# Kernel tuning notes

Measured on AMD Instinct MI355X. Metric: run time of the kernel, lower is better.

Reference implementation:

```python
import jax, jax.numpy as jnp
import numpy as np

DIM = 768      # model dim (c_s)
C_PAIR = 128   # pair channels (c_z)
H = 16         # heads
C = DIM // H   # per-head dim (48)
INF = 1e8
EPS = 1e-5


def _ln(x, w=None, b=None):
    mu = jnp.mean(x, axis=-1, keepdims=True)
    var = jnp.mean(jnp.square(x - mu), axis=-1, keepdims=True)
    y = (x - mu) * jax.lax.rsqrt(var + EPS)
    if w is not None:
        y = y * w
    if b is not None:
        y = y + b
    return y


def setup_inputs() -> dict:
    key = jax.random.key(0)
    ks = jax.random.split(key, 12)
    B, S, N = 1, 2, 1024
    sd = 1.0 / np.sqrt(DIM)
    return {
        "single_repr": jax.random.normal(ks[0], (B, S, N, DIM), jnp.float32),
        "single_proj": jax.random.normal(ks[1], (B, S, N, DIM), jnp.float32),
        "pair_repr": jax.random.normal(ks[2], (B, N, N, C_PAIR), jnp.float32),
        "mask": jnp.ones((B, N), jnp.float32),
        # AdaLN params: LN(a) has no affine; LN(s) is scale-only; gate Linear + skip LinearNoBias
        "adaln_s_w": jnp.ones((DIM,), jnp.float32),
        "adaln_gate_w": (jax.random.normal(ks[3], (DIM, DIM), jnp.float32) * sd),
        "adaln_gate_b": jnp.zeros((DIM,), jnp.float32),
        "adaln_skip_w": (jax.random.normal(ks[4], (DIM, DIM), jnp.float32) * sd),
        # Attention params (q/k/v no bias, sigmoid gate linear, output linear)
        "wq": jax.random.normal(ks[5], (DIM, DIM), jnp.float32) * sd,
        "wk": jax.random.normal(ks[6], (DIM, DIM), jnp.float32) * sd,
        "wv": jax.random.normal(ks[7], (DIM, DIM), jnp.float32) * sd,
        "w_gate": jax.random.normal(ks[8], (DIM, DIM), jnp.float32) * sd,
        "b_gate": jnp.ones((DIM,), jnp.float32),
        "wo": jax.random.normal(ks[9], (DIM, DIM), jnp.float32) * sd,
        "bo": jnp.zeros((DIM,), jnp.float32),
        # proj_pair_bias: LayerNorm(c_pair) + LinearNoBias(c_pair, H)
        "pair_ln_w": jnp.ones((C_PAIR,), jnp.float32),
        "pair_ln_b": jnp.zeros((C_PAIR,), jnp.float32),
        "w_pair": jax.random.normal(ks[10], (C_PAIR, H), jnp.float32) / np.sqrt(C_PAIR),
        # output gating linear (bias initialized to -2 as in the module)
        "w_out": jax.random.normal(ks[11], (DIM, DIM), jnp.float32) * sd,
        "b_out": jnp.full((DIM,), -2.0, jnp.float32),
    }


def reference(single_repr, single_proj, pair_repr, mask,
              adaln_s_w, adaln_gate_w, adaln_gate_b, adaln_skip_w,
              wq, wk, wv, w_gate, b_gate, wo, bo,
              pair_ln_w, pair_ln_b, w_pair, w_out, b_out):
    B, S, N, _ = single_repr.shape
    # AdaLN input gating: a = sigmoid(Lin(LN_scale(s))) * LN(a) + LinNoBias(LN_scale(s))
    a = _ln(single_repr)
    s = _ln(single_proj, adaln_s_w)
    a = jax.nn.sigmoid(s @ adaln_gate_w + adaln_gate_b) * a + s @ adaln_skip_w
    # Biases: mask_bias [B,1,1,1,N]; pair_bias [B,1,H,N,N]
    mask_bias = (INF * (mask - 1.0))[:, None, None, None, :]
    pair_bias = _ln(pair_repr, pair_ln_w, pair_ln_b) @ w_pair      # [B,N,N,H]
    pair_bias = jnp.transpose(pair_bias, (0, 3, 1, 2))[:, None]    # [B,1,H,N,N]
    # Multi-head attention with fused biases
    q = (a @ wq).reshape(B, S, N, H, C)
    k = (a @ wk).reshape(B, S, N, H, C)
    v = (a @ wv).reshape(B, S, N, H, C)
    scale = 1.0 / np.sqrt(C)
    scores = jnp.einsum('bsqhc,bskhc->bshqk', q, k) * scale + mask_bias + pair_bias
    attn = jax.nn.softmax(scores, axis=-1)
    o = jnp.einsum('bshqk,bskhc->bsqhc', attn, v).reshape(B, S, N, DIM)
    # sigmoid gating on attention output, then output projection
    o = o * jax.nn.sigmoid(a @ w_gate + b_gate)
    o = o @ wo + bo
    # final sigmoid output gating (input_gating=True)
    out = jax.nn.sigmoid(o @ w_out + b_out) * o
    return out
```

## Files before the change

### kernel.cpp

```cpp
#include <hip/hip_runtime.h>

#define NROWS 2048
#define NN    1024
#define DIMM  768
#define HEADS 16
#define CH    48
#define CPAIR 128

typedef unsigned short u16;
typedef unsigned int   u32;
typedef __attribute__((ext_vector_type(8))) short short8;
typedef __attribute__((ext_vector_type(4))) float f32x4;

__device__ __forceinline__ float sigm(float x){ return 1.0f/(1.0f+__expf(-x)); }
__device__ __forceinline__ u16 f2bf(float x){
    u32 u = __float_as_uint(x);
    u32 r = u + 0x7FFFu + ((u>>16)&1u);
    return (u16)(r>>16);
}
__device__ __forceinline__ float bf2f(u16 h){ return __uint_as_float(((u32)h)<<16); }
__device__ __forceinline__ void bfsplit(float x, u16& hi, u16& lo){
    hi = f2bf(x);
    lo = f2bf(x - bf2f(hi));
}

__global__ __launch_bounds__(256) void k_pre(
    const float* __restrict__ srep, const float* __restrict__ sproj,
    const float* __restrict__ sw, float* __restrict__ a_ln,
    u16* __restrict__ shi, u16* __restrict__ slo,
    const float* __restrict__ w0, const float* __restrict__ w1,
    const float* __restrict__ w2, const float* __restrict__ w3,
    const float* __restrict__ w4, const float* __restrict__ w5,
    const float* __restrict__ w6, const float* __restrict__ w7,
    u16* __restrict__ wt,
    const float* __restrict__ plnw, const float* __restrict__ plnb,
    const float* __restrict__ wp, float* __restrict__ wpc,
    float* __restrict__ csb)
{
    __shared__ float tile[64][68];
    __shared__ float red[16];
    int bid = blockIdx.x, t = threadIdx.x;
    if (bid < 2048){
        int r = bid;
        const float* xa = srep  + (size_t)r*DIMM;
        const float* xs = sproj + (size_t)r*DIMM;
        float va[3], vs[3];
        float sa=0.f,qa=0.f,ss=0.f,qs=0.f;
        #pragma unroll
        for (int i=0;i<3;i++){ float x=xa[t+256*i]; va[i]=x; sa+=x; qa+=x*x; }
        #pragma unroll
        for (int i=0;i<3;i++){ float x=xs[t+256*i]; vs[i]=x; ss+=x; qs+=x*x; }
        #pragma unroll
        for (int off=32; off>=1; off>>=1){
            sa += __shfl_xor(sa,off); qa += __shfl_xor(qa,off);
            ss += __shfl_xor(ss,off); qs += __shfl_xor(qs,off);
        }
        int w = t>>6;
        if ((t&63)==0){ red[w*4+0]=sa; red[w*4+1]=qa; red[w*4+2]=ss; red[w*4+3]=qs; }
        __syncthreads();
        sa = red[0]+red[4]+red[8]+red[12];
        qa = red[1]+red[5]+red[9]+red[13];
        ss = red[2]+red[6]+red[10]+red[14];
        qs = red[3]+red[7]+red[11]+red[15];
        float mua=sa*(1.f/768.f), mus=ss*(1.f/768.f);
        float rva=rsqrtf(fmaxf(qa*(1.f/768.f)-mua*mua,0.f)+1e-5f);
        float rvs=rsqrtf(fmaxf(qs*(1.f/768.f)-mus*mus,0.f)+1e-5f);
        #pragma unroll
        for (int i=0;i<3;i++){
            int c=t+256*i;
            size_t idx=(size_t)r*DIMM+c;
            a_ln[idx]=(va[i]-mua)*rva;
            float sv=(vs[i]-mus)*rvs*sw[c];
            u16 h,l; bfsplit(sv,h,l);
            shi[idx]=h; slo[idx]=l;
        }
        return;
    }
    if (bid < 3200){
        int b = bid - 2048;
        int n0 = (b%12)*64, k0 = ((b/12)%12)*64, z = b/144;
        const float* src;
        switch(z){
            case 0: src=w0; break; case 1: src=w1; break;
            case 2: src=w2; break; case 3: src=w3; break;
            case 4: src=w4; break; case 5: src=w5; break;
            case 6: src=w6; break; default: src=w7; break;
        }
        #pragma unroll
        for (int it=0; it<4; it++){
            int idx = t + it*256;
            int kr = idx>>4, nc = (idx&15)*4;
            float4 v = *(const float4*)(src + (size_t)(k0+kr)*DIMM + n0+nc);
            *(float4*)(&tile[kr][nc]) = v;
        }
        __syncthreads();
        u16* wth = wt + (size_t)z*2*589824;
        u16* wtl = wth + 589824;
        #pragma unroll
        for (int it=0; it<4; it++){
            int idx = t + it*256;
            int nr = idx>>4, kc = (idx&15)*4;
            ushort4 h4, l4;
            u16 h,l;
            bfsplit(tile[kc+0][nr],h,l); h4.x=h; l4.x=l;
            bfsplit(tile[kc+1][nr],h,l); h4.y=h; l4.y=l;
            bfsplit(tile[kc+2][nr],h,l); h4.z=h; l4.z=l;
            bfsplit(tile[kc+3][nr],h,l); h4.w=h; l4.w=l;
            size_t o = (size_t)(n0+nr)*DIMM + k0+kc;
            *(ushort4*)(wth + o) = h4;
            *(ushort4*)(wtl + o) = l4;
        }
        return;
    }
    for (int i=t;i<2048;i+=256) wpc[i] = plnw[i>>4]*wp[i];
    if (t<16){
        float cs=0.f,b0=0.f;
        for (int c=0;c<128;c++){ cs += plnw[c]*wp[c*16+t]; b0 += plnb[c]*wp[c*16+t]; }
        csb[t]=cs; csb[16+t]=b0;
    }
}

template<int NB>
__device__ __forceinline__ void gemm_tile(
    const u16* __restrict__ Ahp, const u16* __restrict__ Alp,
    const u16* __restrict__ B0h, const u16* __restrict__ B0l,
    const u16* __restrict__ B1h, const u16* __restrict__ B1l,
    int m0, int n0, int t,
    u16 (&lA)[2][128][40], u16 (&lB)[NB][2][64][40],
    f32x4 (&acc)[NB][2][4])
{
    int lane = t&63, w = t>>6;
    int fr = lane&15, fg = lane>>4;
    for (int k0=0; k0<DIMM; k0+=32){
        #pragma unroll
        for (int it=0; it<4; it++){
            int s = t + it*256;
            int pl = s>>9, s2 = s&511;
            int row = s2>>2, seg = (s2&3)*8;
            *(int4*)(&lA[pl][row][seg]) =
                *(const int4*)((pl?Alp:Ahp) + (size_t)(m0+row)*DIMM + k0 + seg);
        }
        #pragma unroll
        for (int i=0;i<NB;i++){
            const u16* bh = i ? B1h : B0h;
            const u16* bl = i ? B1l : B0l;
            #pragma unroll
            for (int it=0; it<2; it++){
                int s = t + it*256;
                int pl = s>>8, s2 = s&255;
                int row = s2>>2, seg = (s2&3)*8;
                *(int4*)(&lB[i][pl][row][seg]) =
                    *(const int4*)((pl?bl:bh) + (size_t)(n0+row)*DIMM + k0 + seg);
            }
        }
        __syncthreads();
        short8 a_h0 = *(const short8*)(&lA[0][w*32+fr][fg*8]);
        short8 a_h1 = *(const short8*)(&lA[0][w*32+16+fr][fg*8]);
        short8 a_l0 = *(const short8*)(&lA[1][w*32+fr][fg*8]);
        short8 a_l1 = *(const short8*)(&lA[1][w*32+16+fr][fg*8]);
        #pragma unroll
        for (int nf=0;nf<4;nf++){
            #pragma unroll
            for (int i=0;i<NB;i++){
                short8 b_h = *(const short8*)(&lB[i][0][nf*16+fr][fg*8]);
                short8 b_l = *(const short8*)(&lB[i][1][nf*16+fr][fg*8]);
                acc[i][0][nf] = __builtin_amdgcn_mfma_f32_16x16x32_bf16(a_h0, b_h, acc[i][0][nf], 0,0,0);
                acc[i][0][nf] = __builtin_amdgcn_mfma_f32_16x16x32_bf16(a_h0, b_l, acc[i][0][nf], 0,0,0);
                acc[i][0][nf] = __builtin_amdgcn_mfma_f32_16x16x32_bf16(a_l0, b_h, acc[i][0][nf], 0,0,0);
                acc[i][1][nf] = __builtin_amdgcn_mfma_f32_16x16x32_bf16(a_h1, b_h, acc[i][1][nf], 0,0,0);
                acc[i][1][nf] = __builtin_amdgcn_mfma_f32_16x16x32_bf16(a_h1, b_l, acc[i][1][nf], 0,0,0);
                acc[i][1][nf] = __builtin_amdgcn_mfma_f32_16x16x32_bf16(a_l1, b_h, acc[i][1][nf], 0,0,0);
            }
        }
        __syncthreads();
    }
}

__device__ __forceinline__ void fma16(float yc, const float* __restrict__ wrow,
                                      float acc[16])
{
    const float4* wr = (const float4*)wrow;
    float4 w0=wr[0], w1=wr[1], w2=wr[2], w3=wr[3];
    acc[0]+=yc*w0.x;  acc[1]+=yc*w0.y;  acc[2]+=yc*w0.z;  acc[3]+=yc*w0.w;
    acc[4]+=yc*w1.x;  acc[5]+=yc*w1.y;  acc[6]+=yc*w1.z;  acc[7]+=yc*w1.w;
    acc[8]+=yc*w2.x;  acc[9]+=yc*w2.y;  acc[10]+=yc*w2.z; acc[11]+=yc*w2.w;
    acc[12]+=yc*w3.x; acc[13]+=yc*w3.y; acc[14]+=yc*w3.z; acc[15]+=yc*w3.w;
}

__global__ __launch_bounds__(256) void k_pb_g1(
    const float* __restrict__ pair, const float* __restrict__ wpc,
    const float* __restrict__ csb, const float* __restrict__ mask,
    u16* __restrict__ pb,
    const u16* __restrict__ shi, const u16* __restrict__ slo,
    const u16* __restrict__ gwh, const u16* __restrict__ gwl,
    const u16* __restrict__ skh, const u16* __restrict__ skl,
    const float* __restrict__ gate_b, const float* __restrict__ a_ln,
    u16* __restrict__ ahi, u16* __restrict__ alo)
{
    __shared__ u16 lA[2][128][40];
    __shared__ u16 lB[2][2][64][40];
    int bid = blockIdx.x, t = threadIdx.x;
    if (bid < 4096){
        int row = bid*256 + t;
        int j = row & (NN-1);
        const float4* x4 = (const float4*)(pair + (size_t)row*CPAIR);
        float s=0.f, sq=0.f;
        float acc[16];
        #pragma unroll
        for (int h=0;h<16;h++) acc[h]=0.f;
        #pragma unroll 4
        for (int i=0;i<32;i++){
            float4 v = x4[i];
            s  += v.x+v.y+v.z+v.w;
            sq += v.x*v.x+v.y*v.y+v.z*v.z+v.w*v.w;
            fma16(v.x, wpc + (4*i+0)*16, acc);
            fma16(v.y, wpc + (4*i+1)*16, acc);
            fma16(v.z, wpc + (4*i+2)*16, acc);
            fma16(v.w, wpc + (4*i+3)*16, acc);
        }
        float mu = s*(1.f/128.f);
        float rs = rsqrtf(fmaxf(sq*(1.f/128.f)-mu*mu,0.f)+1e-5f);
        float mb = 1e8f*(mask[j]-1.f);
        #pragma unroll
        for (int h=0;h<16;h++){
            float outv = (acc[h]-mu*csb[h])*rs + csb[16+h] + mb;
            pb[((size_t)h<<20) + row] = f2bf(outv);
        }
        return;
    }
    int b = bid - 4096;
    int m0 = (b&15)*128, n0 = (b>>4)*64;
    int lane = t&63, w = t>>6;
    int fr = lane&15, fg = lane>>4;
    f32x4 acc[2][2][4];
    #pragma unroll
    for (int i=0;i<2;i++)
        #pragma unroll
        for (int mf=0;mf<2;mf++)
            #pragma unroll
            for (int nf=0;nf<4;nf++) acc[i][mf][nf] = (f32x4){0.f,0.f,0.f,0.f};
    gemm_tile<2>(shi, slo, gwh, gwl, skh, skl, m0, n0, t, lA, lB, acc);
    #pragma unroll
    for (int mf=0;mf<2;mf++){
        #pragma unroll
        for (int nf=0;nf<4;nf++){
            #pragma unroll
            for (int r=0;r<4;r++){
                int row = m0 + w*32 + mf*16 + fg*4 + r;
                int col = n0 + nf*16 + fr;
                size_t idx = (size_t)row*DIMM + col;
                float c0 = acc[0][mf][nf][r];
                float c1 = acc[1][mf][nf][r];
                float v = sigm(c0 + gate_b[col]) * a_ln[idx] + c1;
                u16 h,l; bfsplit(v,h,l); ahi[idx]=h; alo[idx]=l;
            }
        }
    }
}

template<int EPI>
__global__ __launch_bounds__(256) void k_gemm(
    const u16* __restrict__ Ahp, const u16* __restrict__ Alp,
    const u16* __restrict__ B0h, const u16* __restrict__ B0l,
    const float* __restrict__ e0,
    float* __restrict__ o0,
    u16* __restrict__ oh, u16* __restrict__ ol)
{
    __shared__ u16 lA[2][128][40];
    __shared__ u16 lB[1][2][64][40];
    int m0 = blockIdx.x*128, n0 = blockIdx.y*64;
    int t = threadIdx.x, lane = t&63, w = t>>6;
    int fr = lane&15, fg = lane>>4;
    f32x4 acc[1][2][4];
    #pragma unroll
    for (int mf=0;mf<2;mf++)
        #pragma unroll
        for (int nf=0;nf<4;nf++) acc[0][mf][nf] = (f32x4){0.f,0.f,0.f,0.f};

    gemm_tile<1>(Ahp, Alp, B0h, B0l, nullptr, nullptr, m0, n0, t, lA, lB, acc);

    #pragma unroll
    for (int mf=0;mf<2;mf++){
        #pragma unroll
        for (int nf=0;nf<4;nf++){
            #pragma unroll
            for (int r=0;r<4;r++){
                int row = m0 + w*32 + mf*16 + fg*4 + r;
                int col = n0 + nf*16 + fr;
                size_t idx = (size_t)row*DIMM + col;
                float c0 = acc[0][mf][nf][r];
                if (EPI==3){
                    float v = c0 + e0[col];
                    u16 h,l; bfsplit(v,h,l); oh[idx]=h; ol[idx]=l;
                } else {
                    float o2v = bf2f(Ahp[idx]) + bf2f(Alp[idx]);
                    o0[idx] = sigm(c0 + e0[col]) * o2v;
                }
            }
        }
    }
}

__global__ __launch_bounds__(256) void k_gemm_qkvg(
    const u16* __restrict__ Ahp, const u16* __restrict__ Alp,
    const u16* __restrict__ wqh, const u16* __restrict__ wql,
    const u16* __restrict__ wkh, const u16* __restrict__ wkl,
    const u16* __restrict__ wvh, const u16* __restrict__ wvl,
    const u16* __restrict__ wgh, const u16* __restrict__ wgl,
    const float* __restrict__ bgate,
    u16* __restrict__ qah, u16* __restrict__ qal,
    u16* __restrict__ kah, u16* __restrict__ kal,
    u16* __restrict__ vth, u16* __restrict__ vtl,
    float* __restrict__ g)
{
    __shared__ u16 lA[2][128][40];
    __shared__ u16 lB[2][2][64][40];
    int m0 = blockIdx.x*128, n0 = blockIdx.y*64;
    int z = blockIdx.z;
    const u16* B0h = z ? wvh : wqh;
    const u16* B0l = z ? wvl : wql;
    const u16* B1h = z ? wgh : wkh;
    const u16* B1l = z ? wgl : wkl;
    int t = threadIdx.x, lane = t&63, w = t>>6;
    int fr = lane&15, fg = lane>>4;
    f32x4 acc[2][2][4];
    #pragma unroll
    for (int i=0;i<2;i++)
        #pragma unroll
        for (int mf=0;mf<2;mf++)
            #pragma unroll
            for (int nf=0;nf<4;nf++) acc[i][mf][nf] = (f32x4){0.f,0.f,0.f,0.f};

    gemm_tile<2>(Ahp, Alp, B0h, B0l, B1h, B1l, m0, n0, t, lA, lB, acc);

    #pragma unroll
    for (int mf=0;mf<2;mf++){
        #pragma unroll
        for (int nf=0;nf<4;nf++){
            #pragma unroll
            for (int r=0;r<4;r++){
                int row = m0 + w*32 + mf*16 + fg*4 + r;
                int col = n0 + nf*16 + fr;
                size_t idx = (size_t)row*DIMM + col;
                int s2 = row>>10, n = row&(NN-1);
                int hh2 = col/CH, cc = col-hh2*CH;
                float c0 = acc[0][mf][nf][r];
                float c1 = acc[1][mf][nf][r];
                if (z==0){
                    size_t pidx = ((size_t)(s2*HEADS+hh2)*NN + n)*CH + cc;
                    u16 hx,lx;
                    bfsplit(c0*0.14433756729740643f, hx,lx);
                    qah[pidx]=hx; qal[pidx]=lx;
                    bfsplit(c1,hx,lx);
                    kah[pidx]=hx; kal[pidx]=lx;
                } else {
                    size_t vidx = ((size_t)(s2*HEADS+hh2)*CH + cc)*NN + n;
                    u16 hx,lx; bfsplit(c0,hx,lx);
                    vth[vidx]=hx; vtl[vidx]=lx;
                    g[idx] = sigm(c1 + bgate[col]);
                }
            }
        }
    }
}

__global__ __launch_bounds__(256) void k_attn(
    const u16* __restrict__ qah, const u16* __restrict__ qal,
    const u16* __restrict__ kah, const u16* __restrict__ kal,
    const u16* __restrict__ vth, const u16* __restrict__ vtl,
    const u16* __restrict__ pb, const float* __restrict__ g,
    u16* __restrict__ oghi, u16* __restrict__ oglo)
{
    __shared__ u16 lQh[64][72], lQl[64][72], lKh[64][72], lKl[64][72];
    __shared__ u16 lVh[48][72], lVl[48][72];
    __shared__ u16 lP[4][16][72];
    int t = threadIdx.x, lane = t&63, w = t>>6;
    int fr = lane&15, fg = lane>>4;
    int m0 = blockIdx.x*64;
    int sh = blockIdx.y, s = sh>>4, h = sh&15;
    size_t qkbase = (size_t)sh*NN*CH;
    size_t vbase  = (size_t)sh*CH*NN;

    {
        int row = t>>2, which = t&3;
        u16* dst = (which==0)? &lQh[row][48] : (which==1)? &lQl[row][48] :
                   (which==2)? &lKh[row][48] : &lKl[row][48];
        *(int4*)dst     = make_int4(0,0,0,0);
        *(int4*)(dst+8) = make_int4(0,0,0,0);
    }
    {
        const u16* src0 = qah + qkbase + (size_t)m0*CH;
        const u16* src1 = qal + qkbase + (size_t)m0*CH;
        #pragma unroll
        for (int it=0; it<3; it++){
            int sid = t + it*256;
            int plane = sid>=384; int s2 = plane ? sid-384 : sid;
            int row = s2/6, seg = s2-row*6;
            int4 v = *(const int4*)((plane?src1:src0) + row*CH + seg*8);
            u16 (*dq)[72] = plane? lQl : lQh;
            *(int4*)(&dq[row][seg*8]) = v;
        }
    }
    __syncthreads();
    short8 aqh0 = *(const short8*)(&lQh[w*16+fr][fg*8]);
    short8 aqh1 = *(const short8*)(&lQh[w*16+fr][32+fg*8]);
    short8 aql0 = *(const short8*)(&lQl[w*16+fr][fg*8]);
    short8 aql1 = *(const short8*)(&lQl[w*16+fr][32+fg*8]);

    f32x4 acc_o[3];
    #pragma unroll
    for (int i=0;i<3;i++) acc_o[i]=(f32x4){0.f,0.f,0.f,0.f};
    float m[4], l[4];
    #pragma unroll
    for (int r=0;r<4;r++){ m[r]=-3e38f; l[r]=0.f; }
    int qrow_base = m0 + w*16 + fg*4;
    const u16* pbq = pb + ((size_t)h<<20) + (size_t)qrow_base*NN + fr;

    for (int kt=0; kt<16; kt++){
        int k0 = kt*64;
        int4 kreg[3], vreg[3];
        const u16* ksrc0 = kah + qkbase + (size_t)k0*CH;
        const u16* ksrc1 = kal + qkbase + (size_t)k0*CH;
        const u16* vsrc0 = vth + vbase + k0;
        const u16* vsrc1 = vtl + vbase + k0;
        #pragma unroll
        for (int it=0; it<3; it++){
            int sid = t + it*256;
            int plane = sid>=384; int s2 = plane ? sid-384 : sid;
            int row = s2/6, seg = s2-row*6;
            kreg[it] = *(const int4*)((plane?ksrc1:ksrc0) + row*CH + seg*8);
            int rowv = s2>>3, segv = s2&7;
            vreg[it] = *(const int4*)((plane?vsrc1:vsrc0) + (size_t)rowv*NN + segv*8);
        }
        u16 pbv[4][4];
        #pragma unroll
        for (int r=0;r<4;r++)
            #pragma unroll
            for (int nf=0;nf<4;nf++)
                pbv[r][nf] = pbq[(size_t)r*NN + k0 + nf*16];
        __syncthreads();
        #pragma unroll
        for (int it=0; it<3; it++){
            int sid = t + it*256;
            int plane = sid>=384; int s2 = plane ? sid-384 : sid;
            int row = s2/6, seg = s2-row*6;
            u16 (*dk)[72] = plane? lKl : lKh;
            *(int4*)(&dk[row][seg*8]) = kreg[it];
            int rowv = s2>>3, segv = s2&7;
            u16 (*dv)[72] = plane? lVl : lVh;
            *(int4*)(&dv[rowv][segv*8]) = vreg[it];
        }
        __syncthreads();
        f32x4 sc[4];
        #pragma unroll
        for (int nf=0;nf<4;nf++){
            short8 bh0 = *(const short8*)(&lKh[nf*16+fr][fg*8]);
            short8 bh1 = *(const short8*)(&lKh[nf*16+fr][32+fg*8]);
            short8 bl0 = *(const short8*)(&lKl[nf*16+fr][fg*8]);
            short8 bl1 = *(const short8*)(&lKl[nf*16+fr][32+fg*8]);
            f32x4 a = (f32x4){0.f,0.f,0.f,0.f};
            a = __builtin_amdgcn_mfma_f32_16x16x32_bf16(aqh0, bh0, a, 0,0,0);
            a = __builtin_amdgcn_mfma_f32_16x16x32_bf16(aqh1, bh1, a, 0,0,0);
            a = __builtin_amdgcn_mfma_f32_16x16x32_bf16(aqh0, bl0, a, 0,0,0);
            a = __builtin_amdgcn_mfma_f32_16x16x32_bf16(aqh1, bl1, a, 0,0,0);
            a = __builtin_amdgcn_mfma_f32_16x16x32_bf16(aql0, bh0, a, 0,0,0);
            a = __builtin_amdgcn_mfma_f32_16x16x32_bf16(aql1, bh1, a, 0,0,0);
            sc[nf]=a;
        }
        float mn[4];
        #pragma unroll
        for (int r=0;r<4;r++){
            float v0 = sc[0][r]+bf2f(pbv[r][0]);
            float v1 = sc[1][r]+bf2f(pbv[r][1]);
            float v2 = sc[2][r]+bf2f(pbv[r][2]);
            float v3 = sc[3][r]+bf2f(pbv[r][3]);
            sc[0][r]=v0; sc[1][r]=v1; sc[2][r]=v2; sc[3][r]=v3;
            float mx = fmaxf(fmaxf(v0,v1),fmaxf(v2,v3));
            mx = fmaxf(mx, __shfl_xor(mx,1,64));
            mx = fmaxf(mx, __shfl_xor(mx,2,64));
            mx = fmaxf(mx, __shfl_xor(mx,4,64));
            mx = fmaxf(mx, __shfl_xor(mx,8,64));
            mn[r]=mx;
        }
        #pragma unroll
        for (int r=0;r<4;r++){
            float mnew = fmaxf(m[r], mn[r]);
            float corr = __expf(m[r]-mnew);
            m[r]=mnew;
            float ps=0.f;
            #pragma unroll
            for (int nf=0;nf<4;nf++){
                float p = __expf(sc[nf][r]-mnew);
                u16 pu = f2bf(p);
                ps += bf2f(pu);
                lP[w][fg*4+r][nf*16+fr] = pu;
            }
            l[r] = l[r]*corr + ps;
            acc_o[0][r]*=corr; acc_o[1][r]*=corr; acc_o[2][r]*=corr;
        }
        short8 pa0 = *(const short8*)(&lP[w][fr][fg*8]);
        short8 pa1 = *(const short8*)(&lP[w][fr][32+fg*8]);
        #pragma unroll
        for (int cf=0;cf<3;cf++){
            short8 vh0 = *(const short8*)(&lVh[cf*16+fr][fg*8]);
            short8 vh1 = *(const short8*)(&lVh[cf*16+fr][32+fg*8]);
            short8 vl0 = *(const short8*)(&lVl[cf*16+fr][fg*8]);
            short8 vl1 = *(const short8*)(&lVl[cf*16+fr][32+fg*8]);
            acc_o[cf] = __builtin_amdgcn_mfma_f32_16x16x32_bf16(pa0, vh0, acc_o[cf], 0,0,0);
            acc_o[cf] = __builtin_amdgcn_mfma_f32_16x16x32_bf16(pa1, vh1, acc_o[cf], 0,0,0);
            acc_o[cf] = __builtin_amdgcn_mfma_f32_16x16x32_bf16(pa0, vl0, acc_o[cf], 0,0,0);
            acc_o[cf] = __builtin_amdgcn_mfma_f32_16x16x32_bf16(pa1, vl1, acc_o[cf], 0,0,0);
        }
    }
    float rl[4];
    #pragma unroll
    for (int r=0;r<4;r++){
        float lv = l[r];
        lv += __shfl_xor(lv,1,64);
        lv += __shfl_xor(lv,2,64);
        lv += __shfl_xor(lv,4,64);
        lv += __shfl_xor(lv,8,64);
        rl[r] = 1.f/lv;
    }
    #pragma unroll
    for (int cf=0;cf<3;cf++){
        #pragma unroll
        for (int r=0;r<4;r++){
            size_t orow = ((size_t)(s*NN + m0 + w*16 + fg*4 + r))*DIMM + h*CH + cf*16 + fr;
            float val = acc_o[cf][r]*rl[r] * g[orow];
            u16 hh,ll; bfsplit(val,hh,ll);
            oghi[orow]=hh; oglo[orow]=ll;
        }
    }
}

extern "C" void kernel_launch(void* const* d_in, const int* in_sizes, int n_in,
                              void* d_out, int out_size, void* d_ws, size_t ws_size,
                              hipStream_t stream)
{
    const float* srep   = (const float*)d_in[0];
    const float* sproj  = (const float*)d_in[1];
    const float* pair   = (const float*)d_in[2];
    const float* mask   = (const float*)d_in[3];
    const float* s_w    = (const float*)d_in[4];
    const float* gate_w = (const float*)d_in[5];
    const float* gate_b = (const float*)d_in[6];
    const float* skip_w = (const float*)d_in[7];
    const float* wq     = (const float*)d_in[8];
    const float* wk     = (const float*)d_in[9];
    const float* wv     = (const float*)d_in[10];
    const float* w_gate = (const float*)d_in[11];
    const float* b_gate = (const float*)d_in[12];
    const float* wo     = (const float*)d_in[13];
    const float* bo     = (const float*)d_in[14];
    const float* plnw   = (const float*)d_in[15];
    const float* plnb   = (const float*)d_in[16];
    const float* w_pair = (const float*)d_in[17];
    const float* w_out  = (const float*)d_in[18];
    const float* b_out  = (const float*)d_in[19];
    float* out = (float*)d_out;

    const size_t T  = (size_t)NROWS*DIMM;
    const size_t W  = (size_t)DIMM*DIMM;
    const size_t PB = (size_t)HEADS*NN*NN;

    char* p = (char*)d_ws;
    float* a_ln = (float*)p; p += T*4;
    float* g    = (float*)p; p += T*4;
    float* wpc  = (float*)p; p += 2048*4;
    float* csb  = (float*)p; p += 32*4;
    u16* shi  = (u16*)p; p += T*2;
    u16* slo  = (u16*)p; p += T*2;
    u16* ahi  = (u16*)p; p += T*2;
    u16* alo  = (u16*)p; p += T*2;
    u16* oghi = (u16*)p; p += T*2;
    u16* oglo = (u16*)p; p += T*2;
    u16* o2hi = (u16*)p; p += T*2;
    u16* o2lo = (u16*)p; p += T*2;
    u16* qah  = (u16*)p; p += T*2;
    u16* qal  = (u16*)p; p += T*2;
    u16* kah  = (u16*)p; p += T*2;
    u16* kal  = (u16*)p; p += T*2;
    u16* vth  = (u16*)p; p += T*2;
    u16* vtl  = (u16*)p; p += T*2;
    u16* pbias= (u16*)p; p += PB*2;
    u16* wt   = (u16*)p; p += 16*W*2;

    #define WH(i) (wt + (size_t)(i)*2*W)
    #define WL(i) (wt + (size_t)(i)*2*W + W)

    k_pre<<<2048+1152+1, 256, 0, stream>>>(
        srep, sproj, s_w, a_ln, shi, slo,
        gate_w, skip_w, wq, wk, wv, w_gate, wo, w_out, wt,
        plnw, plnb, w_pair, wpc, csb);

    k_pb_g1<<<4096+192, 256, 0, stream>>>(
        pair, wpc, csb, mask, pbias,
        shi, slo, WH(0), WL(0), WH(1), WL(1), gate_b, a_ln, ahi, alo);

    k_gemm_qkvg<<<dim3(NROWS/128, DIMM/64, 2), 256, 0, stream>>>(
        ahi, alo, WH(2), WL(2), WH(3), WL(3), WH(4), WL(4), WH(5), WL(5),
        b_gate, qah, qal, kah, kal, vth, vtl, g);

    k_attn<<<dim3(NN/64, 2*HEADS), 256, 0, stream>>>(
        qah, qal, kah, kal, vth, vtl, pbias, g, oghi, oglo);

    dim3 gg(NROWS/128, DIMM/64);
    k_gemm<3><<<gg, 256, 0, stream>>>(oghi, oglo, WH(6), WL(6), bo,
                                      nullptr, o2hi, o2lo);
    k_gemm<4><<<gg, 256, 0, stream>>>(o2hi, o2lo, WH(7), WL(7), b_out,
                                      out, nullptr, nullptr);
    #undef WH
    #undef WL
}
```

Baseline: 372.7 us.

## Load attention Q/K/V MFMA fragments directly from global, drop LDS staging

The attention kernel no longer stages Q, K and V tiles through shared memory with two barriers per key tile. Each wave now reads its MFMA operand fragments straight from global memory (relying on L1/L2 for reuse across the four waves), and zero-fills the padded channel half with a predicate. This removes the LDS round-trip and block-wide syncs, but each wave now issues its own uncoalesced-ish global loads, and latency is no longer hidden by a register prefetch.

```diff
diff --git a/kernel.cpp b/kernel.cpp
--- a/kernel.cpp
+++ b/kernel.cpp
@@ -23,6 +23,7 @@
     hi = f2bf(x);
     lo = f2bf(x - bf2f(hi));
 }
+__device__ __forceinline__ short8 zero8(){ short8 z = {0,0,0,0,0,0,0,0}; return z; }
 
 __global__ __launch_bounds__(256) void k_pre(
     const float* __restrict__ srep, const float* __restrict__ sproj,
@@ -371,8 +372,6 @@
     const u16* __restrict__ pb, const float* __restrict__ g,
     u16* __restrict__ oghi, u16* __restrict__ oglo)
 {
-    __shared__ u16 lQh[64][72], lQl[64][72], lKh[64][72], lKl[64][72];
-    __shared__ u16 lVh[48][72], lVl[48][72];
     __shared__ u16 lP[4][16][72];
     int t = threadIdx.x, lane = t&63, w = t>>6;
     int fr = lane&15, fg = lane>>4;
@@ -380,32 +379,14 @@
     int sh = blockIdx.y, s = sh>>4, h = sh&15;
     size_t qkbase = (size_t)sh*NN*CH;
     size_t vbase  = (size_t)sh*CH*NN;
-
-    {
-        int row = t>>2, which = t&3;
-        u16* dst = (which==0)? &lQh[row][48] : (which==1)? &lQl[row][48] :
-                   (which==2)? &lKh[row][48] : &lKl[row][48];
-        *(int4*)dst     = make_int4(0,0,0,0);
-        *(int4*)(dst+8) = make_int4(0,0,0,0);
-    }
-    {
-        const u16* src0 = qah + qkbase + (size_t)m0*CH;
-        const u16* src1 = qal + qkbase + (size_t)m0*CH;
-        #pragma unroll
-        for (int it=0; it<3; it++){
-            int sid = t + it*256;
-            int plane = sid>=384; int s2 = plane ? sid-384 : sid;
-            int row = s2/6, seg = s2-row*6;
-            int4 v = *(const int4*)((plane?src1:src0) + row*CH + seg*8);
-            u16 (*dq)[72] = plane? lQl : lQh;
-            *(int4*)(&dq[row][seg*8]) = v;
-        }
-    }
-    __syncthreads();
-    short8 aqh0 = *(const short8*)(&lQh[w*16+fr][fg*8]);
-    short8 aqh1 = *(const short8*)(&lQh[w*16+fr][32+fg*8]);
-    short8 aql0 = *(const short8*)(&lQl[w*16+fr][fg*8]);
-    short8 aql1 = *(const short8*)(&lQl[w*16+fr][32+fg*8]);
+    bool lo_ok = (fg < 2);
+
+    const u16* qrow_h = qah + qkbase + (size_t)(m0 + w*16 + fr)*CH;
+    const u16* qrow_l = qal + qkbase + (size_t)(m0 + w*16 + fr)*CH;
+    short8 aqh0 = *(const short8*)(qrow_h + fg*8);
+    short8 aql0 = *(const short8*)(qrow_l + fg*8);
+    short8 aqh1 = lo_ok ? *(const short8*)(qrow_h + 32 + fg*8) : zero8();
+    short8 aql1 = lo_ok ? *(const short8*)(qrow_l + 32 + fg*8) : zero8();
 
     f32x4 acc_o[3];
     #pragma unroll
@@ -418,46 +399,15 @@
 
     for (int kt=0; kt<16; kt++){
         int k0 = kt*64;
-        int4 kreg[3], vreg[3];
-        const u16* ksrc0 = kah + qkbase + (size_t)k0*CH;
-        const u16* ksrc1 = kal + qkbase + (size_t)k0*CH;
-        const u16* vsrc0 = vth + vbase + k0;
-        const u16* vsrc1 = vtl + vbase + k0;
-        #pragma unroll
-        for (int it=0; it<3; it++){
-            int sid = t + it*256;
-            int plane = sid>=384; int s2 = plane ? sid-384 : sid;
-            int row = s2/6, seg = s2-row*6;
-            kreg[it] = *(const int4*)((plane?ksrc1:ksrc0) + row*CH + seg*8);
-            int rowv = s2>>3, segv = s2&7;
-            vreg[it] = *(const int4*)((plane?vsrc1:vsrc0) + (size_t)rowv*NN + segv*8);
-        }
-        u16 pbv[4][4];
-        #pragma unroll
-        for (int r=0;r<4;r++)
-            #pragma unroll
-            for (int nf=0;nf<4;nf++)
-                pbv[r][nf] = pbq[(size_t)r*NN + k0 + nf*16];
-        __syncthreads();
-        #pragma unroll
-        for (int it=0; it<3; it++){
-            int sid = t + it*256;
-            int plane = sid>=384; int s2 = plane ? sid-384 : sid;
-            int row = s2/6, seg = s2-row*6;
-            u16 (*dk)[72] = plane? lKl : lKh;
-            *(int4*)(&dk[row][seg*8]) = kreg[it];
-            int rowv = s2>>3, segv = s2&7;
-            u16 (*dv)[72] = plane? lVl : lVh;
-            *(int4*)(&dv[rowv][segv*8]) = vreg[it];
-        }
-        __syncthreads();
         f32x4 sc[4];
         #pragma unroll
         for (int nf=0;nf<4;nf++){
-            short8 bh0 = *(const short8*)(&lKh[nf*16+fr][fg*8]);
-            short8 bh1 = *(const short8*)(&lKh[nf*16+fr][32+fg*8]);
-            short8 bl0 = *(const short8*)(&lKl[nf*16+fr][fg*8]);
-            short8 bl1 = *(const short8*)(&lKl[nf*16+fr][32+fg*8]);
+            const u16* krow_h = kah + qkbase + (size_t)(k0 + nf*16 + fr)*CH;
+            const u16* krow_l = kal + qkbase + (size_t)(k0 + nf*16 + fr)*CH;
+            short8 bh0 = *(const short8*)(krow_h + fg*8);
+            short8 bl0 = *(const short8*)(krow_l + fg*8);
+            short8 bh1 = lo_ok ? *(const short8*)(krow_h + 32 + fg*8) : zero8();
+            short8 bl1 = lo_ok ? *(const short8*)(krow_l + 32 + fg*8) : zero8();
             f32x4 a = (f32x4){0.f,0.f,0.f,0.f};
             a = __builtin_amdgcn_mfma_f32_16x16x32_bf16(aqh0, bh0, a, 0,0,0);
             a = __builtin_amdgcn_mfma_f32_16x16x32_bf16(aqh1, bh1, a, 0,0,0);
@@ -467,6 +417,12 @@
             a = __builtin_amdgcn_mfma_f32_16x16x32_bf16(aql1, bh1, a, 0,0,0);
             sc[nf]=a;
         }
+        u16 pbv[4][4];
+        #pragma unroll
+        for (int r=0;r<4;r++)
+            #pragma unroll
+            for (int nf=0;nf<4;nf++)
+                pbv[r][nf] = pbq[(size_t)r*NN + k0 + nf*16];
         float mn[4];
         #pragma unroll
         for (int r=0;r<4;r++){
@@ -502,10 +458,12 @@
         short8 pa1 = *(const short8*)(&lP[w][fr][32+fg*8]);
         #pragma unroll
         for (int cf=0;cf<3;cf++){
-            short8 vh0 = *(const short8*)(&lVh[cf*16+fr][fg*8]);
-            short8 vh1 = *(const short8*)(&lVh[cf*16+fr][32+fg*8]);
-            short8 vl0 = *(const short8*)(&lVl[cf*16+fr][fg*8]);
-            short8 vl1 = *(const short8*)(&lVl[cf*16+fr][32+fg*8]);
+            const u16* vrow_h = vth + vbase + (size_t)(cf*16+fr)*NN + k0;
+            const u16* vrow_l = vtl + vbase + (size_t)(cf*16+fr)*NN + k0;
+            short8 vh0 = *(const short8*)(vrow_h + fg*8);
+            short8 vh1 = *(const short8*)(vrow_h + 32 + fg*8);
+            short8 vl0 = *(const short8*)(vrow_l + fg*8);
+            short8 vl1 = *(const short8*)(vrow_l + 32 + fg*8);
             acc_o[cf] = __builtin_amdgcn_mfma_f32_16x16x32_bf16(pa0, vh0, acc_o[cf], 0,0,0);
             acc_o[cf] = __builtin_amdgcn_mfma_f32_16x16x32_bf16(pa1, vh1, acc_o[cf], 0,0,0);
             acc_o[cf] = __builtin_amdgcn_mfma_f32_16x16x32_bf16(pa0, vl0, acc_o[cf], 0,0,0);
```

After: 400.8 us. 1.08x slower.
